# Kernel tuning notes

Hardware: AMD Instinct MI355X
Metric: run time of the kernel (lower is better)

Reference implementation:

```python
import jax, jax.numpy as jnp
import numpy as np

B, S, DM = 2, 2048, 1024
H, DH = 16, 64
SCALE = jnp.sqrt(jnp.float32(DH))  # dot_scale = sqrt(dim_head)


def setup_inputs() -> dict:
    key = jax.random.key(0)
    ks = jax.random.split(key, 9)
    std = 1.0 / np.sqrt(DM)
    x = jax.random.normal(ks[0], (B, S, DM), dtype=jnp.float32)
    Wq = jax.random.uniform(ks[1], (DM, DM), jnp.float32, -std, std)
    bq = jax.random.uniform(ks[2], (DM,), jnp.float32, -std, std)
    Wk = jax.random.uniform(ks[3], (DM, DM), jnp.float32, -std, std)
    bk = jax.random.uniform(ks[4], (DM,), jnp.float32, -std, std)
    Wv = jax.random.uniform(ks[5], (DM, DM), jnp.float32, -std, std)
    bv = jax.random.uniform(ks[6], (DM,), jnp.float32, -std, std)
    Wo = jax.random.uniform(ks[7], (DM, DM), jnp.float32, -std, std)
    bo = jax.random.uniform(ks[8], (DM,), jnp.float32, -std, std)
    # causal mask: 1 = masked (future positions), broadcast over batch
    causal = jnp.triu(jnp.ones((S, S), dtype=jnp.int32), k=1)
    attention_mask = jnp.broadcast_to(causal, (B, S, S))
    return {"x": x, "Wq": Wq, "bq": bq, "Wk": Wk, "bk": bk,
            "Wv": Wv, "bv": bv, "Wo": Wo, "bo": bo,
            "attention_mask": attention_mask}


def reference(x, Wq, bq, Wk, bk, Wv, bv, Wo, bo, attention_mask):
    # Linear layers (torch nn.Linear: y = x @ W^T + b)
    q = (x @ Wq.T + bq).reshape(B, S, H, DH).transpose(0, 2, 1, 3)  # (B,H,S,DH)
    k = (x @ Wk.T + bk).reshape(B, S, H, DH).transpose(0, 2, 1, 3)  # (B,H,S,DH)
    v = (x @ Wv.T + bv).reshape(B, S, H, DH).transpose(0, 2, 1, 3)  # (B,H,S,DH)
    # scores: (B,H,S,S), then mask==1 -> -inf, softmax over last dim
    scores = jnp.einsum('bhsd,bhtd->bhst', q, k) / SCALE
    mask = attention_mask[:, None, :, :]  # (B,1,S,S)
    scores = jnp.where(mask == 1, -jnp.inf, scores)
    attn = jax.nn.softmax(scores, axis=-1)
    # dropout is identity in eval mode
    ctx = jnp.einsum('bhst,bhtd->bshd', attn, v).reshape(B, S, H * DH)
    return ctx @ Wo.T + bo
```

## Files before the change

### kernel.cpp

```cpp
#include <hip/hip_runtime.h>
#include <stdint.h>

typedef unsigned short u16;
typedef __attribute__((ext_vector_type(8))) short bf16x8;
typedef __attribute__((ext_vector_type(4))) float f32x4;
typedef __attribute__((ext_vector_type(16))) float f32x16;
typedef __attribute__((ext_vector_type(4))) uint32_t u32x4;

#define BATCH 2
#define S_LEN 2048
#define DMODEL 1024
#define NH 16
#define DHEAD 64
#define MTOT 4096
#define QSCALE 0.18033688011112042f

#define GL2LDS(g, l) \
  __builtin_amdgcn_global_load_lds((const __attribute__((address_space(1))) void*)(g), \
                                   (__attribute__((address_space(3))) void*)(l), 16, 0, 0)

__device__ __forceinline__ u16 f2bf(float x) {
  union { float f; uint32_t u; } v; v.f = x;
  uint32_t r = v.u + 0x7fffu + ((v.u >> 16) & 1u);
  return (u16)(r >> 16);
}

__device__ __forceinline__ uint32_t cvtpk_bf16(float lo, float hi) {
  uint32_t r;
  asm("v_cvt_pk_bf16_f32 %0, %1, %2" : "=v"(r) : "v"(lo), "v"(hi));
  return r;
}

struct CvtArgs {
  const float* src[5];
  u16* dst[5];
};

__global__ __launch_bounds__(256) void cvt_all(CvtArgs a) {
  int bx = blockIdx.x;
  int region, off;
  if (bx < 4096) { region = 0; off = bx; }
  else { region = 1 + ((bx - 4096) >> 10); off = (bx - 4096) & 1023; }
  const float* s = a.src[region];
  u16* d = a.dst[region];
  int i = (off * 256 + threadIdx.x) * 4;
  float4 v = *(const float4*)(s + i);
  uint2 pk;
  pk.x = (uint32_t)f2bf(v.x) | ((uint32_t)f2bf(v.y) << 16);
  pk.y = (uint32_t)f2bf(v.z) | ((uint32_t)f2bf(v.w) << 16);
  *(uint2*)(d + i) = pk;
}

__device__ __forceinline__ void gemm_body(const u16* __restrict__ A,
                                          const u16* __restrict__ W,
                                          const float* __restrict__ bias,
                                          void* __restrict__ out,
                                          int mode, float scale,
                                          int m0, int n0) {
  __shared__ u16 As[2][128 * 32];
  __shared__ u16 Bs[2][128 * 32];
  const int tid = threadIdx.x;
  const int wave = tid >> 6, lane = tid & 63;
  const int wm = (wave >> 1) * 64, wn = (wave & 1) * 64;
  const int quad = lane >> 4, l15 = lane & 15;

  const int row0 = tid >> 2, g0 = ((tid & 3) ^ (row0 & 3)) * 8;
  const int row1 = (tid + 256) >> 2, g1 = ((tid & 3) ^ (row1 & 3)) * 8;
  const int lb0 = wave * 512;
  const int lb1 = 2048 + wave * 512;
  const int xk = (quad ^ (l15 & 3)) * 8;

  f32x4 acc[4][4] = {};

#define GSTAGE(kt_, pb)                                                     \
  do {                                                                      \
    GL2LDS(A + (size_t)(m0 + row0) * DMODEL + (kt_) + g0, &As[pb][0] + lb0);\
    GL2LDS(A + (size_t)(m0 + row1) * DMODEL + (kt_) + g1, &As[pb][0] + lb1);\
    GL2LDS(W + (size_t)(n0 + row0) * DMODEL + (kt_) + g0, &Bs[pb][0] + lb0);\
    GL2LDS(W + (size_t)(n0 + row1) * DMODEL + (kt_) + g1, &Bs[pb][0] + lb1);\
  } while (0)

  GSTAGE(0, 0);
  for (int t = 0; t < 32; ++t) {
    const int p = t & 1;
    __syncthreads();
    if (t < 31) GSTAGE((t + 1) * 32, p ^ 1);
    bf16x8 af[4], bfr[4];
#pragma unroll
    for (int bi = 0; bi < 4; ++bi)
      af[bi] = *(const bf16x8*)(&As[p][(wm + bi * 16 + l15) * 32 + xk]);
#pragma unroll
    for (int bj = 0; bj < 4; ++bj)
      bfr[bj] = *(const bf16x8*)(&Bs[p][(wn + bj * 16 + l15) * 32 + xk]);
#pragma unroll
    for (int bi = 0; bi < 4; ++bi)
#pragma unroll
      for (int bj = 0; bj < 4; ++bj)
        acc[bi][bj] = __builtin_amdgcn_mfma_f32_16x16x32_bf16(af[bi], bfr[bj], acc[bi][bj], 0, 0, 0);
  }
#undef GSTAGE

#pragma unroll
  for (int bi = 0; bi < 4; ++bi) {
#pragma unroll
    for (int bj = 0; bj < 4; ++bj) {
      int n = n0 + wn + bj * 16 + l15;
      float bval = bias[n];
#pragma unroll
      for (int r = 0; r < 4; ++r) {
        int m = m0 + wm + bi * 16 + quad * 4 + r;
        float v = (acc[bi][bj][r] + bval) * scale;
        u16 bvu = f2bf(v);
        int b = m >> 11, s = m & 2047;
        int h = n >> 6, d = n & 63;
        size_t bh = (size_t)(b * NH + h);
        if (mode == 1)
          ((u16*)out)[(bh * S_LEN + s) * DHEAD + d] = bvu;
        else
          ((u16*)out)[((bh * 256 + (s >> 3)) * 64 + d) * 8 + (s & 7)] = bvu;
      }
    }
  }
}

struct QKVArgs {
  const u16* w[3];
  const float* b[3];
  u16* o[3];
};

__global__ __launch_bounds__(256, 3) void qkv_gemm(const u16* __restrict__ xb, QKVArgs a) {
  int s = blockIdx.x;
  int xcd = s & 7, idx = s >> 3;
  int xx = idx & 3, yy = (idx >> 2) & 7, z = idx >> 5;
  int nt = (xcd & 1) * 4 + xx;
  int mt = (xcd >> 1) * 8 + yy;
  int mode = (z == 2) ? 2 : 1;
  float scale = (z == 0) ? QSCALE : 1.0f;
  gemm_body(xb, a.w[z], a.b[z], a.o[z], mode, scale, mt * 128, nt * 128);
}

__global__ __launch_bounds__(256, 3) void out_gemm(const u16* __restrict__ A,
                                                   const u16* __restrict__ W,
                                                   const float* __restrict__ bias,
                                                   float* __restrict__ out) {
  int sb = blockIdx.x;
  int xcd = sb & 7, idx = sb >> 3;
  int xx = idx & 7, yy = idx >> 3;
  const int n0 = ((xcd & 1) * 8 + xx) * 64;
  const int m0 = ((xcd >> 1) * 8 + yy) * 128;

  __shared__ u16 As[2][128 * 32];
  __shared__ u16 Bs[2][64 * 32];
  const int tid = threadIdx.x;
  const int wave = tid >> 6, lane = tid & 63;
  const int wm = (wave >> 1) * 64, wn = (wave & 1) * 32;
  const int quad = lane >> 4, l15 = lane & 15;

  const int row0 = tid >> 2, g0 = ((tid & 3) ^ (row0 & 3)) * 8;
  const int row1 = (tid + 256) >> 2, g1 = ((tid & 3) ^ (row1 & 3)) * 8;
  const int lb0 = wave * 512;
  const int lb1 = 2048 + wave * 512;
  const int xk = (quad ^ (l15 & 3)) * 8;

  f32x4 acc[4][2] = {};

#define OSTAGE(kt_, pb)                                                     \
  do {                                                                      \
    GL2LDS(A + (size_t)(m0 + row0) * DMODEL + (kt_) + g0, &As[pb][0] + lb0);\
    GL2LDS(A + (size_t)(m0 + row1) * DMODEL + (kt_) + g1, &As[pb][0] + lb1);\
    GL2LDS(W + (size_t)(n0 + row0) * DMODEL + (kt_) + g0, &Bs[pb][0] + lb0);\
  } while (0)

  OSTAGE(0, 0);
  for (int t = 0; t < 32; ++t) {
    const int p = t & 1;
    __syncthreads();
    if (t < 31) OSTAGE((t + 1) * 32, p ^ 1);
    bf16x8 af[4], bfr[2];
#pragma unroll
    for (int bi = 0; bi < 4; ++bi)
      af[bi] = *(const bf16x8*)(&As[p][(wm + bi * 16 + l15) * 32 + xk]);
#pragma unroll
    for (int bj = 0; bj < 2; ++bj)
      bfr[bj] = *(const bf16x8*)(&Bs[p][(wn + bj * 16 + l15) * 32 + xk]);
#pragma unroll
    for (int bi = 0; bi < 4; ++bi)
#pragma unroll
      for (int bj = 0; bj < 2; ++bj)
        acc[bi][bj] = __builtin_amdgcn_mfma_f32_16x16x32_bf16(af[bi], bfr[bj], acc[bi][bj], 0, 0, 0);
  }
#undef OSTAGE

#pragma unroll
  for (int bi = 0; bi < 4; ++bi) {
#pragma unroll
    for (int bj = 0; bj < 2; ++bj) {
      int n = n0 + wn + bj * 16 + l15;
      float bval = bias[n];
#pragma unroll
      for (int r = 0; r < 4; ++r) {
        int m = m0 + wm + bi * 16 + quad * 4 + r;
        out[(size_t)m * DMODEL + n] = acc[bi][bj][r] + bval;
      }
    }
  }
}

__global__ __launch_bounds__(256, 4) void attn(const u16* __restrict__ Q,
                                               const u16* __restrict__ Kg,
                                               const u16* __restrict__ Vt8,
                                               u16* __restrict__ ctx,
                                               float* __restrict__ part_o,
                                               float* __restrict__ part_l) {
  __shared__ u16 Kd[2][64 * 64];
  __shared__ u16 Vd[2][64 * 64];
  const int tid = threadIdx.x;
  const int q3 = blockIdx.x >> 8;
  const int t = (blockIdx.x >> 5) & 7;
  const int bh = blockIdx.x & 31;
  const int wave = tid >> 6, lane = tid & 63;
  const int l31 = lane & 31, hi = lane >> 5;
  const size_t base = (size_t)bh * S_LEN * DHEAD;
  const int b = bh >> 4, h = bh & 15;

  int qs, k0, k1, slot = 0;
  if (q3 == 0) { qs = t; k0 = 0; k1 = 2 * t + 1; }
  else {
    qs = 15 - t;
    int half = qs + 1;
    if (q3 == 1) { k0 = 0; k1 = half - 1; }
    else         { k0 = half; k1 = 2 * qs + 1; }
    slot = ((qs - 8) * 2 + (q3 - 1)) * 32 + bh;
  }

#define STAGE(kt_, pb)                                                                   \
  do {                                                                                   \
    _Pragma("unroll")                                                                    \
    for (int i_ = 0; i_ < 2; ++i_) {                                                     \
      int c_ = tid + 256 * i_;                                                           \
      int row_ = c_ >> 3, g_ = ((c_ & 7) ^ (row_ & 7)) * 8;                              \
      GL2LDS(Kg + base + (size_t)((kt_) * 64 + row_) * 64 + g_,                          \
             &Kd[pb][0] + i_ * 2048 + wave * 512);                                       \
      GL2LDS(Vt8 + base + (size_t)((kt_) * 512 + c_) * 8,                                \
             &Vd[pb][0] + i_ * 2048 + wave * 512);                                       \
    }                                                                                    \
  } while (0)

  const int q0 = qs * 128 + wave * 32;
  bf16x8 qf[4];
#pragma unroll
  for (int s = 0; s < 4; ++s)
    qf[s] = *(const bf16x8*)(Q + base + (size_t)(q0 + l31) * DHEAD + s * 16 + hi * 8);

  f32x16 o0 = {}, o1 = {};
  float lp = 0.f;

  STAGE(k0, 0);
  for (int kt = k0; kt <= k1; ++kt) {
    const int p = (kt - k0) & 1;
    __syncthreads();
    if (kt < k1) STAGE(kt + 1, p ^ 1);

    const int kb0 = kt * 64;
    if (kb0 <= q0 + 31) {
      const u16* Kt = &Kd[p][0];
      const u16* Vt = &Vd[p][0];
      f32x16 sa0 = {}, sa1 = {};
#pragma unroll
      for (int s = 0; s < 4; ++s) {
        bf16x8 kf0 = *(const bf16x8*)(&Kt[l31 * 64 + (((s * 2 + hi) ^ (l31 & 7)) * 8)]);
        sa0 = __builtin_amdgcn_mfma_f32_32x32x16_bf16(kf0, qf[s], sa0, 0, 0, 0);
      }
#pragma unroll
      for (int s = 0; s < 4; ++s) {
        bf16x8 kf1 = *(const bf16x8*)(&Kt[(32 + l31) * 64 + (((s * 2 + hi) ^ (l31 & 7)) * 8)]);
        sa1 = __builtin_amdgcn_mfma_f32_32x32x16_bf16(kf1, qf[s], sa1, 0, 0, 0);
      }
      if (kb0 + 63 > q0) {
        const int qg = q0 + l31;
#pragma unroll
        for (int r = 0; r < 16; ++r) {
          int kg = kb0 + (r & 3) + 4 * hi + 8 * (r >> 2);
          if (kg > qg) sa0[r] = -1e30f;
          if (kg + 32 > qg) sa1[r] = -1e30f;
        }
      }
#pragma unroll
      for (int r = 0; r < 16; ++r) { sa0[r] = exp2f(sa0[r]); lp += sa0[r]; }
#pragma unroll
      for (int r = 0; r < 16; ++r) { sa1[r] = exp2f(sa1[r]); lp += sa1[r]; }
      uint32_t P2[2][8];
#pragma unroll
      for (int m = 0; m < 8; ++m) {
        P2[0][m] = cvtpk_bf16(sa0[2 * m], sa0[2 * m + 1]);
        P2[1][m] = cvtpk_bf16(sa1[2 * m], sa1[2 * m + 1]);
      }
#pragma unroll
      for (int n = 0; n < 4; ++n) {
        const int kb = n >> 1, mb = 4 * (n & 1);
        uint32_t A0 = P2[kb][mb], A0p = P2[kb][mb + 1];
        uint32_t A1 = P2[kb][mb + 2], A1p = P2[kb][mb + 3];
        uint32_t X0  = (uint32_t)__shfl_xor((int)A0, 32, 64);
        uint32_t X0p = (uint32_t)__shfl_xor((int)A0p, 32, 64);
        uint32_t X1  = (uint32_t)__shfl_xor((int)A1, 32, 64);
        uint32_t X1p = (uint32_t)__shfl_xor((int)A1p, 32, 64);
        u32x4 pw;
        pw.x = hi ? X1 : A0;
        pw.y = hi ? X1p : A0p;
        pw.z = hi ? A1 : X0;
        pw.w = hi ? A1p : X0p;
        bf16x8 pfv = __builtin_bit_cast(bf16x8, pw);
        bf16x8 vf0 = *(const bf16x8*)(&Vt[((2 * n + hi) * 64 + l31) * 8]);
        bf16x8 vf1 = *(const bf16x8*)(&Vt[((2 * n + hi) * 64 + 32 + l31) * 8]);
        o0 = __builtin_amdgcn_mfma_f32_32x32x16_bf16(pfv, vf0, o0, 0, 0, 0);
        o1 = __builtin_amdgcn_mfma_f32_32x32x16_bf16(pfv, vf1, o1, 0, 0, 0);
      }
    }
  }

  lp += __shfl_xor(lp, 32, 64);

  if (q3 == 0) {
    float inv = 1.0f / lp;
#pragma unroll
    for (int r = 0; r < 16; ++r) {
      int rl = (r & 3) + 4 * hi + 8 * (r >> 2);
      float invr = __shfl(inv, rl, 64);
      int q = q0 + rl;
      size_t rb = ((size_t)b * S_LEN + q) * DMODEL + h * DHEAD;
      ctx[rb + l31] = f2bf(o0[r] * invr);
      ctx[rb + 32 + l31] = f2bf(o1[r] * invr);
    }
  } else {
    float* po = part_o + (size_t)slot * 8192 + (size_t)wave * 32 * 64;
#pragma unroll
    for (int r = 0; r < 16; ++r) {
      int rl = (r & 3) + 4 * hi + 8 * (r >> 2);
      po[rl * 64 + l31] = o0[r];
      po[rl * 64 + 32 + l31] = o1[r];
    }
    if (hi == 0) part_l[(size_t)slot * 128 + wave * 32 + l31] = lp;
  }
#undef STAGE
}

__global__ __launch_bounds__(256) void combine(const float* __restrict__ part_o,
                                               const float* __restrict__ part_l,
                                               u16* __restrict__ ctx) {
  const int pidx = blockIdx.x;
  const int qs8 = pidx >> 5, bh = pidx & 31;
  const int qs = 8 + qs8;
  const int b = bh >> 4, h = bh & 15;
  const float* poA = part_o + (size_t)((qs8 * 2 + 0) * 32 + bh) * 8192;
  const float* poB = part_o + (size_t)((qs8 * 2 + 1) * 32 + bh) * 8192;
  const float* plA = part_l + (size_t)((qs8 * 2 + 0) * 32 + bh) * 128;
  const float* plB = part_l + (size_t)((qs8 * 2 + 1) * 32 + bh) * 128;
  for (int i = threadIdx.x * 4; i < 8192; i += 1024) {
    int row = i >> 6, col = i & 63;
    float4 oa = *(const float4*)(poA + i);
    float4 ob = *(const float4*)(poB + i);
    float inv = 1.0f / (plA[row] + plB[row]);
    uint2 pk;
    pk.x = (uint32_t)f2bf((oa.x + ob.x) * inv) | ((uint32_t)f2bf((oa.y + ob.y) * inv) << 16);
    pk.y = (uint32_t)f2bf((oa.z + ob.z) * inv) | ((uint32_t)f2bf((oa.w + ob.w) * inv) << 16);
    int srow = qs * 128 + row;
    *(uint2*)(ctx + ((size_t)b * S_LEN + srow) * DMODEL + h * DHEAD + col) = pk;
  }
}

extern "C" void kernel_launch(void* const* d_in, const int* in_sizes, int n_in,
                              void* d_out, int out_size, void* d_ws, size_t ws_size,
                              hipStream_t stream) {
  const float* x  = (const float*)d_in[0];
  const float* Wq = (const float*)d_in[1];
  const float* bq = (const float*)d_in[2];
  const float* Wk = (const float*)d_in[3];
  const float* bk = (const float*)d_in[4];
  const float* Wv = (const float*)d_in[5];
  const float* bv = (const float*)d_in[6];
  const float* Wo = (const float*)d_in[7];
  const float* bo = (const float*)d_in[8];
  float* out = (float*)d_out;

  char* ws = (char*)d_ws;
  const size_t MB = 1u << 20;
  u16* xb   = (u16*)(ws + 0);
  u16* ctxb = xb;
  u16* wqb  = (u16*)(ws + 8 * MB);
  u16* wkb  = (u16*)(ws + 10 * MB);
  u16* wvb  = (u16*)(ws + 12 * MB);
  u16* wob  = (u16*)(ws + 14 * MB);
  u16* qb   = (u16*)(ws + 16 * MB);
  u16* kb   = (u16*)(ws + 24 * MB);
  u16* vtb  = (u16*)(ws + 32 * MB);
  float* part_o = (float*)d_out;
  float* part_l = (float*)(ws + 8 * MB);

  CvtArgs c;
  c.src[0] = x;  c.dst[0] = xb;
  c.src[1] = Wq; c.dst[1] = wqb;
  c.src[2] = Wk; c.dst[2] = wkb;
  c.src[3] = Wv; c.dst[3] = wvb;
  c.src[4] = Wo; c.dst[4] = wob;
  cvt_all<<<4096 + 4 * 1024, 256, 0, stream>>>(c);

  QKVArgs a;
  a.w[0] = wqb; a.w[1] = wkb; a.w[2] = wvb;
  a.b[0] = bq;  a.b[1] = bk;  a.b[2] = bv;
  a.o[0] = qb;  a.o[1] = kb;  a.o[2] = vtb;
  qkv_gemm<<<768, 256, 0, stream>>>(xb, a);

  attn<<<768, 256, 0, stream>>>(qb, kb, vtb, ctxb, part_o, part_l);

  combine<<<256, 256, 0, stream>>>(part_o, part_l, ctxb);

  out_gemm<<<512, 256, 0, stream>>>(ctxb, wob, bo, out);
}
```

Measured before the change: 208.6 us.

## Triple-buffer LDS tiles with explicit vmcnt waits in GEMM and attention loops

The QKV GEMM, output GEMM and attention kernels now use three LDS buffers instead of two and prefetch two tiles ahead. The generic __syncthreads is replaced by a manual s_waitcnt vmcnt(N) plus s_barrier, fenced with sched_barrier, so the next tile's async global-to-LDS loads can stay in flight during compute. The aim is to hide more global-load latency behind the MFMA work. In exchange LDS use per block grows by half, which may cut occupancy, especially in the attention kernel. Correctness relies on the hand-counted vmcnt values matching the number of loads issued per stage.

```diff
diff --git a/kernel.cpp b/kernel.cpp
--- a/kernel.cpp
+++ b/kernel.cpp
@@ -18,6 +18,24 @@
 #define GL2LDS(g, l) \
   __builtin_amdgcn_global_load_lds((const __attribute__((address_space(1))) void*)(g), \
                                    (__attribute__((address_space(3))) void*)(l), 16, 0, 0)
+
+#define PIPE_BARRIER(last)                                          \
+  do {                                                              \
+    if (last) asm volatile("s_waitcnt vmcnt(0)" ::: "memory");      \
+    else      asm volatile("s_waitcnt vmcnt(4)" ::: "memory");      \
+    __builtin_amdgcn_sched_barrier(0);                              \
+    __builtin_amdgcn_s_barrier();                                   \
+    __builtin_amdgcn_sched_barrier(0);                              \
+  } while (0)
+
+#define PIPE_BARRIER3(last)                                         \
+  do {                                                              \
+    if (last) asm volatile("s_waitcnt vmcnt(0)" ::: "memory");      \
+    else      asm volatile("s_waitcnt vmcnt(3)" ::: "memory");      \
+    __builtin_amdgcn_sched_barrier(0);                              \
+    __builtin_amdgcn_s_barrier();                                   \
+    __builtin_amdgcn_sched_barrier(0);                              \
+  } while (0)
 
 __device__ __forceinline__ u16 f2bf(float x) {
   union { float f; uint32_t u; } v; v.f = x;
@@ -57,8 +75,8 @@
                                           void* __restrict__ out,
                                           int mode, float scale,
                                           int m0, int n0) {
-  __shared__ u16 As[2][128 * 32];
-  __shared__ u16 Bs[2][128 * 32];
+  __shared__ u16 As[3][128 * 32];
+  __shared__ u16 Bs[3][128 * 32];
   const int tid = threadIdx.x;
   const int wave = tid >> 6, lane = tid & 63;
   const int wm = (wave >> 1) * 64, wn = (wave & 1) * 64;
@@ -81,22 +99,24 @@
   } while (0)
 
   GSTAGE(0, 0);
+  GSTAGE(32, 1);
+  int rb = 0;
   for (int t = 0; t < 32; ++t) {
-    const int p = t & 1;
-    __syncthreads();
-    if (t < 31) GSTAGE((t + 1) * 32, p ^ 1);
+    PIPE_BARRIER(t == 31);
+    if (t < 30) { int st = rb + 2; if (st >= 3) st -= 3; GSTAGE((t + 2) * 32, st); }
     bf16x8 af[4], bfr[4];
 #pragma unroll
     for (int bi = 0; bi < 4; ++bi)
-      af[bi] = *(const bf16x8*)(&As[p][(wm + bi * 16 + l15) * 32 + xk]);
+      af[bi] = *(const bf16x8*)(&As[rb][(wm + bi * 16 + l15) * 32 + xk]);
 #pragma unroll
     for (int bj = 0; bj < 4; ++bj)
-      bfr[bj] = *(const bf16x8*)(&Bs[p][(wn + bj * 16 + l15) * 32 + xk]);
+      bfr[bj] = *(const bf16x8*)(&Bs[rb][(wn + bj * 16 + l15) * 32 + xk]);
 #pragma unroll
     for (int bi = 0; bi < 4; ++bi)
 #pragma unroll
       for (int bj = 0; bj < 4; ++bj)
         acc[bi][bj] = __builtin_amdgcn_mfma_f32_16x16x32_bf16(af[bi], bfr[bj], acc[bi][bj], 0, 0, 0);
+    rb = (rb + 1 == 3) ? 0 : rb + 1;
   }
 #undef GSTAGE
 
@@ -150,8 +170,8 @@
   const int n0 = ((xcd & 1) * 8 + xx) * 64;
   const int m0 = ((xcd >> 1) * 8 + yy) * 128;
 
-  __shared__ u16 As[2][128 * 32];
-  __shared__ u16 Bs[2][64 * 32];
+  __shared__ u16 As[3][128 * 32];
+  __shared__ u16 Bs[3][64 * 32];
   const int tid = threadIdx.x;
   const int wave = tid >> 6, lane = tid & 63;
   const int wm = (wave >> 1) * 64, wn = (wave & 1) * 32;
@@ -173,22 +193,24 @@
   } while (0)
 
   OSTAGE(0, 0);
+  OSTAGE(32, 1);
+  int rb = 0;
   for (int t = 0; t < 32; ++t) {
-    const int p = t & 1;
-    __syncthreads();
-    if (t < 31) OSTAGE((t + 1) * 32, p ^ 1);
+    PIPE_BARRIER3(t == 31);
+    if (t < 30) { int st = rb + 2; if (st >= 3) st -= 3; OSTAGE((t + 2) * 32, st); }
     bf16x8 af[4], bfr[2];
 #pragma unroll
     for (int bi = 0; bi < 4; ++bi)
-      af[bi] = *(const bf16x8*)(&As[p][(wm + bi * 16 + l15) * 32 + xk]);
+      af[bi] = *(const bf16x8*)(&As[rb][(wm + bi * 16 + l15) * 32 + xk]);
 #pragma unroll
     for (int bj = 0; bj < 2; ++bj)
-      bfr[bj] = *(const bf16x8*)(&Bs[p][(wn + bj * 16 + l15) * 32 + xk]);
+      bfr[bj] = *(const bf16x8*)(&Bs[rb][(wn + bj * 16 + l15) * 32 + xk]);
 #pragma unroll
     for (int bi = 0; bi < 4; ++bi)
 #pragma unroll
       for (int bj = 0; bj < 2; ++bj)
         acc[bi][bj] = __builtin_amdgcn_mfma_f32_16x16x32_bf16(af[bi], bfr[bj], acc[bi][bj], 0, 0, 0);
+    rb = (rb + 1 == 3) ? 0 : rb + 1;
   }
 #undef OSTAGE
 
@@ -213,8 +235,8 @@
                                                u16* __restrict__ ctx,
                                                float* __restrict__ part_o,
                                                float* __restrict__ part_l) {
-  __shared__ u16 Kd[2][64 * 64];
-  __shared__ u16 Vd[2][64 * 64];
+  __shared__ u16 Kd[3][64 * 64];
+  __shared__ u16 Vd[3][64 * 64];
   const int tid = threadIdx.x;
   const int q3 = blockIdx.x >> 8;
   const int t = (blockIdx.x >> 5) & 7;
@@ -257,15 +279,16 @@
   float lp = 0.f;
 
   STAGE(k0, 0);
+  STAGE(k0 + 1, 1);
+  int rb = 0;
   for (int kt = k0; kt <= k1; ++kt) {
-    const int p = (kt - k0) & 1;
-    __syncthreads();
-    if (kt < k1) STAGE(kt + 1, p ^ 1);
+    PIPE_BARRIER(kt == k1);
+    if (kt + 2 <= k1) { int st = rb + 2; if (st >= 3) st -= 3; STAGE(kt + 2, st); }
 
     const int kb0 = kt * 64;
     if (kb0 <= q0 + 31) {
-      const u16* Kt = &Kd[p][0];
-      const u16* Vt = &Vd[p][0];
+      const u16* Kt = &Kd[rb][0];
+      const u16* Vt = &Vd[rb][0];
       f32x16 sa0 = {}, sa1 = {};
 #pragma unroll
       for (int s = 0; s < 4; ++s) {
@@ -317,6 +340,7 @@
         o1 = __builtin_amdgcn_mfma_f32_32x32x16_bf16(pfv, vf1, o1, 0, 0, 0);
       }
     }
+    rb = (rb + 1 == 3) ? 0 : rb + 1;
   }
 
   lp += __shfl_xor(lp, 32, 64);
@@ -328,9 +352,9 @@
       int rl = (r & 3) + 4 * hi + 8 * (r >> 2);
       float invr = __shfl(inv, rl, 64);
       int q = q0 + rl;
-      size_t rb = ((size_t)b * S_LEN + q) * DMODEL + h * DHEAD;
-      ctx[rb + l31] = f2bf(o0[r] * invr);
-      ctx[rb + 32 + l31] = f2bf(o1[r] * invr);
+      size_t rb2 = ((size_t)b * S_LEN + q) * DMODEL + h * DHEAD;
+      ctx[rb2 + l31] = f2bf(o0[r] * invr);
+      ctx[rb2 + 32 + l31] = f2bf(o1[r] * invr);
     }
   } else {
     float* po = part_o + (size_t)slot * 8192 + (size_t)wave * 32 * 64;
```

Result: slower. 215.1 us (+3.1%).
